# Kernel tuning notes

Hardware: AMD Instinct MI355X
Metric: run time of the kernel (lower is better)

Reference implementation:

```python
import jax, jax.numpy as jnp
import numpy as np

WINDOW_SIZE = 64  # matches init_kwargs


def _local_allowed_mask(L, window_size):
    # Original torch code: for query i, keys in slice [max(i-w//2,0) : min(i+w//2, L)) are allowed.
    half = window_size // 2
    i = jnp.arange(L)[:, None]
    j = jnp.arange(L)[None, :]
    return (j >= i - half) & (j < i + half)  # [L, L] bool, True = attend


def setup_inputs() -> dict:
    key = jax.random.key(0)
    kq, kk, kv = jax.random.split(key, 3)
    B, L, H, E, D = 4, 2048, 16, 64, 64
    queries = jax.random.normal(kq, (B, L, H, E), dtype=jnp.float32)
    keys = jax.random.normal(kk, (B, L, H, E), dtype=jnp.float32)
    values = jax.random.normal(kv, (B, L, H, D), dtype=jnp.float32)
    attn_mask = jnp.zeros((1,), dtype=bool)  # unused by the module
    return {"queries": queries, "keys": keys, "values": values, "attn_mask": attn_mask}


def reference(queries, keys, values, attn_mask):
    B, L, H, E = queries.shape
    scale = 1.0 / np.sqrt(E).astype(np.float32)
    allowed = _local_allowed_mask(L, WINDOW_SIZE)  # [L, L]
    # Dense scores, as in the original module (einsum 'blhe,bshe->bhls')
    scores = jnp.einsum('blhe,bshe->bhls', queries, keys)
    neg_inf = jnp.asarray(-jnp.inf, dtype=scores.dtype)
    scores = jnp.where(allowed[None, None, :, :], scores, neg_inf)
    A = jax.nn.softmax(scale * scores, axis=-1)  # [B, H, L, S]
    V = jnp.einsum('bhls,bshd->blhd', A, values)  # [B, L, H, D]
    return V
```

## Files before the change

kernel.cpp:

```cpp
#include <hip/hip_runtime.h>


#define B_ 4
#define L_ 2048
#define H_ 16
#define E_ 64
#define D_ 64
#define VT_STRIDE 152

typedef __attribute__((ext_vector_type(8))) short short8;
typedef __attribute__((ext_vector_type(4))) float f32x4;

__device__ __forceinline__ unsigned int f2bf(float x) {
  unsigned int b = __float_as_uint(x);
  b += 0x7fffu + ((b >> 16) & 1u);
  return b >> 16;
}
__device__ __forceinline__ unsigned int pack2(float a, float b) {
  return f2bf(a) | (f2bf(b) << 16);
}
__device__ __forceinline__ short8 pack8(const f32x4& a, const f32x4& b) {
  union { short8 s; uint4 u; } r;
  r.u = make_uint4(pack2(a[0], a[1]), pack2(a[2], a[3]),
                   pack2(b[0], b[1]), pack2(b[2], b[3]));
  return r.s;
}
__device__ __forceinline__ int clampL(int k) {
  return k < 0 ? 0 : (k > (L_ - 1) ? (L_ - 1) : k);
}

__global__ __launch_bounds__(256, 3)
void local_attn_mfma(const float* __restrict__ qg,
                     const float* __restrict__ kg,
                     const float* __restrict__ vg,
                     float* __restrict__ og) {
  __shared__ __align__(16) float Ks32[128 * 64];
  __shared__ __align__(16) unsigned short Vt[64 * VT_STRIDE];

  const int t = threadIdx.x;
  const int q0 = blockIdx.x * 64;
  const int h = blockIdx.y;
  const int b = blockIdx.z;
  const int kstart = q0 - 32;
  const int wave = t >> 6;
  const int lane = t & 63;
  const int col16 = lane & 15;
  const int quad = lane >> 4;

  const int kp = t >> 2;
  const int dq = t & 3;
  f32x4 va[4], vc[4];
  {
    const int k0 = clampL(kstart + 2 * kp);
    const int k1 = clampL(kstart + 2 * kp + 1);
    const float* p0 = vg + ((size_t)(b * L_ + k0) * H_ + h) * D_ + dq * 16;
    const float* p1 = vg + ((size_t)(b * L_ + k1) * H_ + h) * D_ + dq * 16;
    #pragma unroll
    for (int i = 0; i < 4; ++i) va[i] = *(const f32x4*)(p0 + i * 4);
    #pragma unroll
    for (int i = 0; i < 4; ++i) vc[i] = *(const f32x4*)(p1 + i * 4);
  }
  f32x4 qf0, qf1, qf2, qf3;
  {
    const float* pq = qg + ((size_t)(b * L_ + q0 + wave * 16 + col16) * H_ + h) * E_ + quad * 8;
    qf0 = *(const f32x4*)pq;
    qf1 = *(const f32x4*)(pq + 4);
    qf2 = *(const f32x4*)(pq + 32);
    qf3 = *(const f32x4*)(pq + 36);
  }

  #pragma unroll
  for (int it = 0; it < 8; ++it) {
    const int cid = t + it * 256;
    const int row = cid >> 4, ch = cid & 15;
    const int chs = ch ^ (row & 15);
    const int key = clampL(kstart + row);
    const float* src = kg + ((size_t)(b * L_ + key) * H_ + h) * E_ + chs * 4;
    float* dst = &Ks32[(it * 256 + wave * 64) * 4];
    __builtin_amdgcn_global_load_lds(
        (__attribute__((address_space(1))) void*)src,
        (__attribute__((address_space(3))) void*)dst, 16, 0, 0);
  }

  #pragma unroll
  for (int i = 0; i < 4; ++i)
    #pragma unroll
    for (int j = 0; j < 4; ++j) {
      int d = dq * 16 + i * 4 + j;
      *(unsigned int*)&Vt[d * VT_STRIDE + 2 * kp] = pack2(va[i][j], vc[i][j]);
    }
  *(uint2*)&Vt[(t >> 2) * VT_STRIDE + 128 + (t & 3) * 4] = make_uint2(0u, 0u);

  const short8 qa0 = pack8(qf0, qf1);
  const short8 qa1 = pack8(qf2, qf3);

  __syncthreads();

  const int c0 = (2 * quad) ^ col16;
  const int c1 = (2 * quad + 1) ^ col16;
  const int c2 = (2 * quad + 8) ^ col16;
  const int c3 = (2 * quad + 9) ^ col16;
  f32x4 acc[5];
  #pragma unroll
  for (int tt = 0; tt < 5; ++tt) {
    const int krow = wave * 16 + tt * 16 + col16;
    const float* Kr = &Ks32[krow * 64];
    f32x4 k0 = *(const f32x4*)(Kr + c0 * 4);
    f32x4 k1 = *(const f32x4*)(Kr + c1 * 4);
    f32x4 k2 = *(const f32x4*)(Kr + c2 * 4);
    f32x4 k3 = *(const f32x4*)(Kr + c3 * 4);
    short8 kb0 = pack8(k0, k1);
    short8 kb1 = pack8(k2, k3);
    f32x4 c = {0.f, 0.f, 0.f, 0.f};
    c = __builtin_amdgcn_mfma_f32_16x16x32_bf16(kb0, qa0, c, 0, 0, 0);
    c = __builtin_amdgcn_mfma_f32_16x16x32_bf16(kb1, qa1, c, 0, 0, 0);
    acc[tt] = c;
  }

  float mx = -1e30f;
  #pragma unroll
  for (int tt = 0; tt < 5; ++tt)
    #pragma unroll
    for (int r = 0; r < 4; ++r) {
      const int k_loc = tt * 16 + quad * 4 + r;
      const int gkey = kstart + wave * 16 + k_loc;
      const bool ok = (k_loc >= col16) && (k_loc < col16 + 64) &&
                      (gkey >= 0) && (gkey < L_);
      const float v = ok ? acc[tt][r] * 0.125f : -1e30f;
      acc[tt][r] = v;
      mx = fmaxf(mx, v);
    }
  mx = fmaxf(mx, __shfl_xor(mx, 16));
  mx = fmaxf(mx, __shfl_xor(mx, 32));
  float s = 0.f;
  #pragma unroll
  for (int tt = 0; tt < 5; ++tt)
    #pragma unroll
    for (int r = 0; r < 4; ++r) {
      const float e = __expf(acc[tt][r] - mx);
      acc[tt][r] = e;
      s += e;
    }
  s += __shfl_xor(s, 16);
  s += __shfl_xor(s, 32);
  const float inv = 1.0f / s;

  short8 pa[3];
  {
    union { short8 s8; uint4 u4; } w;
    w.u4 = make_uint4(pack2(acc[0][0] * inv, acc[0][1] * inv),
                      pack2(acc[0][2] * inv, acc[0][3] * inv),
                      pack2(acc[1][0] * inv, acc[1][1] * inv),
                      pack2(acc[1][2] * inv, acc[1][3] * inv));
    pa[0] = w.s8;
    w.u4 = make_uint4(pack2(acc[2][0] * inv, acc[2][1] * inv),
                      pack2(acc[2][2] * inv, acc[2][3] * inv),
                      pack2(acc[3][0] * inv, acc[3][1] * inv),
                      pack2(acc[3][2] * inv, acc[3][3] * inv));
    pa[1] = w.s8;
    w.u4 = make_uint4(pack2(acc[4][0] * inv, acc[4][1] * inv),
                      pack2(acc[4][2] * inv, acc[4][3] * inv), 0u, 0u);
    pa[2] = w.s8;
  }

  f32x4 oacc[4];
  #pragma unroll
  for (int nt = 0; nt < 4; ++nt) oacc[nt] = (f32x4){0.f, 0.f, 0.f, 0.f};
  #pragma unroll
  for (int nt = 0; nt < 4; ++nt) {
    const int rowb = (nt * 16 + col16) * VT_STRIDE;
    #pragma unroll
    for (int ks = 0; ks < 3; ++ks) {
      union { short8 s8; uint2 u2[2]; } vb;
      vb.u2[0] = *(const uint2*)&Vt[rowb + wave * 16 + ks * 32 + quad * 4];
      vb.u2[1] = *(const uint2*)&Vt[rowb + wave * 16 + ks * 32 + 16 + quad * 4];
      oacc[nt] = __builtin_amdgcn_mfma_f32_16x16x32_bf16(pa[ks], vb.s8, oacc[nt], 0, 0, 0);
    }
  }

  #pragma unroll
  for (int r = 0; r < 4; ++r) {
    const int q = q0 + wave * 16 + quad * 4 + r;
    float* orow = og + ((size_t)(b * L_ + q) * H_ + h) * D_;
    #pragma unroll
    for (int nt = 0; nt < 4; ++nt)
      orow[nt * 16 + col16] = oacc[nt][r];
  }
}

extern "C" void kernel_launch(void* const* d_in, const int* in_sizes, int n_in,
                              void* d_out, int out_size, void* d_ws, size_t ws_size,
                              hipStream_t stream) {
  const float* q = (const float*)d_in[0];
  const float* k = (const float*)d_in[1];
  const float* v = (const float*)d_in[2];
  float* o = (float*)d_out;
  dim3 grid(L_ / 64, H_, B_);
  local_attn_mfma<<<grid, dim3(256), 0, stream>>>(q, k, v, o);
}
```

Before: 136.7 us.

## Stage V and Q through LDS via async global_load_lds instead of registers

```diff
diff --git a/kernel.cpp b/kernel.cpp
--- a/kernel.cpp
+++ b/kernel.cpp
@@ -6,7 +6,6 @@
 #define H_ 16
 #define E_ 64
 #define D_ 64
-#define VT_STRIDE 152
 
 typedef __attribute__((ext_vector_type(8))) short short8;
 typedef __attribute__((ext_vector_type(4))) float f32x4;
@@ -29,13 +28,14 @@
   return k < 0 ? 0 : (k > (L_ - 1) ? (L_ - 1) : k);
 }
 
-__global__ __launch_bounds__(256, 3)
+__global__ __launch_bounds__(256, 2)
 void local_attn_mfma(const float* __restrict__ qg,
                      const float* __restrict__ kg,
                      const float* __restrict__ vg,
                      float* __restrict__ og) {
   __shared__ __align__(16) float Ks32[128 * 64];
-  __shared__ __align__(16) unsigned short Vt[64 * VT_STRIDE];
+  __shared__ __align__(16) float Vs32[128 * 64];
+  __shared__ __align__(16) float Qs32[64 * 64];
 
   const int t = threadIdx.x;
   const int q0 = blockIdx.x * 64;
@@ -46,28 +46,6 @@
   const int lane = t & 63;
   const int col16 = lane & 15;
   const int quad = lane >> 4;
-
-  const int kp = t >> 2;
-  const int dq = t & 3;
-  f32x4 va[4], vc[4];
-  {
-    const int k0 = clampL(kstart + 2 * kp);
-    const int k1 = clampL(kstart + 2 * kp + 1);
-    const float* p0 = vg + ((size_t)(b * L_ + k0) * H_ + h) * D_ + dq * 16;
-    const float* p1 = vg + ((size_t)(b * L_ + k1) * H_ + h) * D_ + dq * 16;
-    #pragma unroll
-    for (int i = 0; i < 4; ++i) va[i] = *(const f32x4*)(p0 + i * 4);
-    #pragma unroll
-    for (int i = 0; i < 4; ++i) vc[i] = *(const f32x4*)(p1 + i * 4);
-  }
-  f32x4 qf0, qf1, qf2, qf3;
-  {
-    const float* pq = qg + ((size_t)(b * L_ + q0 + wave * 16 + col16) * H_ + h) * E_ + quad * 8;
-    qf0 = *(const f32x4*)pq;
-    qf1 = *(const f32x4*)(pq + 4);
-    qf2 = *(const f32x4*)(pq + 32);
-    qf3 = *(const f32x4*)(pq + 36);
-  }
 
   #pragma unroll
   for (int it = 0; it < 8; ++it) {
@@ -81,36 +59,50 @@
         (__attribute__((address_space(1))) void*)src,
         (__attribute__((address_space(3))) void*)dst, 16, 0, 0);
   }
-
   #pragma unroll
-  for (int i = 0; i < 4; ++i)
-    #pragma unroll
-    for (int j = 0; j < 4; ++j) {
-      int d = dq * 16 + i * 4 + j;
-      *(unsigned int*)&Vt[d * VT_STRIDE + 2 * kp] = pack2(va[i][j], vc[i][j]);
-    }
-  *(uint2*)&Vt[(t >> 2) * VT_STRIDE + 128 + (t & 3) * 4] = make_uint2(0u, 0u);
-
-  const short8 qa0 = pack8(qf0, qf1);
-  const short8 qa1 = pack8(qf2, qf3);
+  for (int it = 0; it < 8; ++it) {
+    const int cid = t + it * 256;
+    const int row = cid >> 4, ch = cid & 15;
+    const int key = clampL(kstart + row);
+    const float* src = vg + ((size_t)(b * L_ + key) * H_ + h) * D_ + ch * 4;
+    float* dst = &Vs32[(it * 256 + wave * 64) * 4];
+    __builtin_amdgcn_global_load_lds(
+        (__attribute__((address_space(1))) void*)src,
+        (__attribute__((address_space(3))) void*)dst, 16, 0, 0);
+  }
+  #pragma unroll
+  for (int it = 0; it < 4; ++it) {
+    const int cid = t + it * 256;
+    const int row = cid >> 4, ch = cid & 15;
+    const int chs = ch ^ (row & 15);
+    const float* src = qg + ((size_t)(b * L_ + q0 + row) * H_ + h) * E_ + chs * 4;
+    float* dst = &Qs32[(it * 256 + wave * 64) * 4];
+    __builtin_amdgcn_global_load_lds(
+        (__attribute__((address_space(1))) void*)src,
+        (__attribute__((address_space(3))) void*)dst, 16, 0, 0);
+  }
 
   __syncthreads();
 
-  const int c0 = (2 * quad) ^ col16;
-  const int c1 = (2 * quad + 1) ^ col16;
-  const int c2 = (2 * quad + 8) ^ col16;
-  const int c3 = (2 * quad + 9) ^ col16;
+  const int s0 = (2 * quad) ^ col16;
+  const int s1 = (2 * quad + 1) ^ col16;
+  const int s2 = (2 * quad + 8) ^ col16;
+  const int s3 = (2 * quad + 9) ^ col16;
+
+  short8 qa0, qa1;
+  {
+    const float* Qr = &Qs32[(wave * 16 + col16) * 64];
+    qa0 = pack8(*(const f32x4*)(Qr + s0 * 4), *(const f32x4*)(Qr + s1 * 4));
+    qa1 = pack8(*(const f32x4*)(Qr + s2 * 4), *(const f32x4*)(Qr + s3 * 4));
+  }
+
   f32x4 acc[5];
   #pragma unroll
   for (int tt = 0; tt < 5; ++tt) {
     const int krow = wave * 16 + tt * 16 + col16;
     const float* Kr = &Ks32[krow * 64];
-    f32x4 k0 = *(const f32x4*)(Kr + c0 * 4);
-    f32x4 k1 = *(const f32x4*)(Kr + c1 * 4);
-    f32x4 k2 = *(const f32x4*)(Kr + c2 * 4);
-    f32x4 k3 = *(const f32x4*)(Kr + c3 * 4);
-    short8 kb0 = pack8(k0, k1);
-    short8 kb1 = pack8(k2, k3);
+    const short8 kb0 = pack8(*(const f32x4*)(Kr + s0 * 4), *(const f32x4*)(Kr + s1 * 4));
+    const short8 kb1 = pack8(*(const f32x4*)(Kr + s2 * 4), *(const f32x4*)(Kr + s3 * 4));
     f32x4 c = {0.f, 0.f, 0.f, 0.f};
     c = __builtin_amdgcn_mfma_f32_16x16x32_bf16(kb0, qa0, c, 0, 0, 0);
     c = __builtin_amdgcn_mfma_f32_16x16x32_bf16(kb1, qa1, c, 0, 0, 0);
@@ -124,8 +116,8 @@
     for (int r = 0; r < 4; ++r) {
       const int k_loc = tt * 16 + quad * 4 + r;
       const int gkey = kstart + wave * 16 + k_loc;
-      const bool ok = (k_loc >= col16) && (k_loc < col16 + 64) &&
-                      (gkey >= 0) && (gkey < L_);
+      const bool ok = ((unsigned)(k_loc - col16) < 64u) &&
+                      ((unsigned)gkey < (unsigned)L_);
       const float v = ok ? acc[tt][r] * 0.125f : -1e30f;
       acc[tt][r] = v;
       mx = fmaxf(mx, v);
@@ -168,13 +160,18 @@
   for (int nt = 0; nt < 4; ++nt) oacc[nt] = (f32x4){0.f, 0.f, 0.f, 0.f};
   #pragma unroll
   for (int nt = 0; nt < 4; ++nt) {
-    const int rowb = (nt * 16 + col16) * VT_STRIDE;
+    const int dim = nt * 16 + col16;
     #pragma unroll
     for (int ks = 0; ks < 3; ++ks) {
-      union { short8 s8; uint2 u2[2]; } vb;
-      vb.u2[0] = *(const uint2*)&Vt[rowb + wave * 16 + ks * 32 + quad * 4];
-      vb.u2[1] = *(const uint2*)&Vt[rowb + wave * 16 + ks * 32 + 16 + quad * 4];
-      oacc[nt] = __builtin_amdgcn_mfma_f32_16x16x32_bf16(pa[ks], vb.s8, oacc[nt], 0, 0, 0);
+      f32x4 va, vb4;
+      #pragma unroll
+      for (int j = 0; j < 8; ++j) {
+        int slot = wave * 16 + ks * 32 + ((j >> 2) << 4) + quad * 4 + (j & 3);
+        if (ks == 2 && j >= 4) slot &= 127;
+        const float vv = Vs32[slot * 64 + dim];
+        if (j < 4) va[j] = vv; else vb4[j - 4] = vv;
+      }
+      oacc[nt] = __builtin_amdgcn_mfma_f32_16x16x32_bf16(pa[ks], pack8(va, vb4), oacc[nt], 0, 0, 0);
     }
   }
 
```

After: 138.4 us. About the same (+1.3%).
